# Performance work log

Measured on AMD Instinct MI355X. Metric: run time of the kernel, lower is better.

## Reference

```python
import jax, jax.numpy as jnp
import numpy as np
from jax import lax

C = 64
EPS = 1e-5


def _layernorm_c(x, g, b):
    # LayerNorm over channel dim of NCHW tensor (matches nn.LayerNorm([C]) applied on NHWC)
    mu = jnp.mean(x, axis=1, keepdims=True)
    var = jnp.var(x, axis=1, keepdims=True)
    xn = (x - mu) * lax.rsqrt(var + EPS)
    return xn * g[None, :, None, None] + b[None, :, None, None]


def _conv1x1(x, w, b):
    # w: [O, I]
    return jnp.einsum('bihw,oi->bohw', x, w) + b[None, :, None, None]


def _dwconv3x3(x, w, b):
    # depthwise 3x3, w: [C, 3, 3]
    k = w[:, None, :, :]  # OIHW with I=1
    y = lax.conv_general_dilated(x, k, (1, 1), 'SAME',
                                 feature_group_count=w.shape[0],
                                 dimension_numbers=('NCHW', 'OIHW', 'NCHW'))
    return y + b[None, :, None, None]


def setup_inputs() -> dict:
    key = jax.random.key(0)
    ks = jax.random.split(key, 24)
    s = 0.02
    d = {}
    d['x'] = jax.random.normal(ks[0], (4, C, 64, 64), dtype=jnp.float32)
    # CTA params
    d['cta_ln_g'] = jnp.ones((C,), jnp.float32)
    d['cta_ln_b'] = jnp.zeros((C,), jnp.float32)
    d['q_w'] = jax.random.normal(ks[1], (C, C), jnp.float32) * s
    d['q_b'] = jnp.zeros((C,), jnp.float32)
    d['k_w'] = jax.random.normal(ks[2], (C, 3, 3), jnp.float32) * s
    d['k_b'] = jnp.zeros((C,), jnp.float32)
    d['v_w'] = jax.random.normal(ks[3], (C, 3, 3), jnp.float32) * s
    d['v_b'] = jnp.zeros((C,), jnp.float32)
    d['cta_out_w'] = jax.random.normal(ks[4], (C, C), jnp.float32) * s
    d['cta_out_b'] = jnp.zeros((C,), jnp.float32)
    # NLE params
    d['nle_ln_g'] = jnp.ones((C,), jnp.float32)
    d['nle_ln_b'] = jnp.zeros((C,), jnp.float32)
    d['b1_w1'] = jax.random.normal(ks[5], (2 * C, C), jnp.float32) * s
    d['b1_b1'] = jnp.zeros((2 * C,), jnp.float32)
    d['b1_w2'] = jax.random.normal(ks[6], (2 * C, 3, 3), jnp.float32) * s
    d['b1_b2'] = jnp.zeros((2 * C,), jnp.float32)
    d['b2_w1'] = jax.random.normal(ks[7], (2 * C, C), jnp.float32) * s
    d['b2_b1'] = jnp.zeros((2 * C,), jnp.float32)
    d['b2_w2'] = jax.random.normal(ks[8], (2 * C, 3, 3), jnp.float32) * s
    d['b2_b2'] = jnp.zeros((2 * C,), jnp.float32)
    d['nle_out_w'] = jax.random.normal(ks[9], (C, 2 * C), jnp.float32) * s
    d['nle_out_b'] = jnp.zeros((C,), jnp.float32)
    return d


def csam_forward(x, cta_ln_g, cta_ln_b, q_w, q_b, k_w, k_b, v_w, v_b, cta_out_w, cta_out_b,
                 nle_ln_g, nle_ln_b, b1_w1, b1_b1, b1_w2, b1_b2, b2_w1, b2_b1, b2_w2, b2_b2,
                 nle_out_w, nle_out_b):
    B, Cc, H, W = x.shape
    scale = jnp.sqrt(jnp.float32(Cc))
    # --- CTA ---
    xn = _layernorm_c(x, cta_ln_g, cta_ln_b)
    q = _conv1x1(xn, q_w, q_b).reshape(B, Cc, H * W)      # [B,C,N]
    k = _dwconv3x3(xn, k_w, k_b).reshape(B, Cc, H * W)    # [B,C,N]
    v = _dwconv3x3(xn, v_w, v_b).reshape(B, Cc, H * W)    # [B,C,N]
    attn = jnp.einsum('bcn,bcm->bnm', q, k) / scale        # [B,N,N]
    attn = jax.nn.softmax(attn, axis=-1)
    out = jnp.einsum('bnm,bcm->bcn', attn, v).reshape(B, Cc, H, W)
    x_att = _conv1x1(out, cta_out_w, cta_out_b) + x
    # --- NLE ---
    xn2 = _layernorm_c(x_att, nle_ln_g, nle_ln_b)
    br1 = jax.nn.gelu(_dwconv3x3(_conv1x1(xn2, b1_w1, b1_b1), b1_w2, b1_b2), approximate=False)
    br2 = jax.nn.gelu(_dwconv3x3(_conv1x1(xn2, b2_w1, b2_b1), b2_w2, b2_b2), approximate=False)
    nle = _conv1x1(br1 * br2, nle_out_w, nle_out_b)
    return nle + x_att


def reference(x, cta_ln_g, cta_ln_b, q_w, q_b, k_w, k_b, v_w, v_b, cta_out_w, cta_out_b,
              nle_ln_g, nle_ln_b, b1_w1, b1_b1, b1_w2, b1_b2, b2_w1, b2_b1, b2_w2, b2_b2,
              nle_out_w, nle_out_b):
    return csam_forward(x, cta_ln_g, cta_ln_b, q_w, q_b, k_w, k_b, v_w, v_b, cta_out_w, cta_out_b,
                        nle_ln_g, nle_ln_b, b1_w1, b1_b1, b1_w2, b1_b2, b2_w1, b2_b1, b2_w2, b2_b2,
                        nle_out_w, nle_out_b)
```

## Files before the change

### kernel.cpp

```cpp
#include <hip/hip_runtime.h>
#include <hip/hip_bf16.h>
#include <math.h>

#define NPIX 4096
#define CH 64
#define BATCH 4
#define NSPLIT 4

typedef __attribute__((ext_vector_type(8))) short short8;
typedef __attribute__((ext_vector_type(4))) float f32x4;
typedef __attribute__((ext_vector_type(4))) unsigned short us4;
typedef __attribute__((ext_vector_type(4))) unsigned int u32x4;

static __device__ __forceinline__ unsigned short f2bf(float f) {
  union { float f; unsigned u; } v; v.f = f;
  unsigned u = v.u;
  unsigned r = u + 0x7FFF + ((u >> 16) & 1);
  return (unsigned short)(r >> 16);
}
static __device__ __forceinline__ float bf2f(unsigned short u) {
  union { unsigned u; float f; } v; v.u = ((unsigned)u) << 16; return v.f;
}
static __device__ __forceinline__ unsigned cvtpk(float lo, float hi) {
  unsigned r;
  asm("v_cvt_pk_bf16_f32 %0, %1, %2" : "=v"(r) : "v"(lo), "v"(hi));
  return r;
}

__global__ __launch_bounds__(256) void k_ln_q(
    const float* __restrict__ x, const float* __restrict__ lg, const float* __restrict__ lb,
    const float* __restrict__ qw, const float* __restrict__ qb,
    float* __restrict__ xn, unsigned short* __restrict__ Q)
{
  __shared__ float xT[64][64];
  __shared__ unsigned short xB[64][64];
  int tid = threadIdx.x, px = tid & 63, g4 = tid >> 6;
  int idx0 = blockIdx.x * 64;
  int idx = idx0 + px;
  int b = idx >> 12, p = idx & 4095;
  const float* xb = x + (size_t)b * CH * NPIX + p;
  for (int j = 0; j < 16; ++j) { int c = 16 * g4 + j; xT[c][px] = xb[(size_t)c * NPIX]; }
  __syncthreads();
  float xv[64]; float s = 0.f;
#pragma unroll
  for (int c = 0; c < 64; ++c) { xv[c] = xT[c][px]; s += xv[c]; }
  float mu = s * (1.f / 64.f), vs = 0.f;
#pragma unroll
  for (int c = 0; c < 64; ++c) { float d = xv[c] - mu; vs += d * d; }
  float rs = rsqrtf(vs * (1.f / 64.f) + 1e-5f);
#pragma unroll
  for (int c = 0; c < 64; ++c) xv[c] = (xv[c] - mu) * rs * lg[c] + lb[c];

  float* xnb = xn + (size_t)b * CH * NPIX + p;
#define LNQ_WR(C0)                                                             \
  {                                                                            \
    unsigned short t[16];                                                      \
    _Pragma("unroll") for (int j = 0; j < 16; ++j) {                           \
      float v = xv[C0 + j];                                                    \
      xnb[(size_t)(C0 + j) * NPIX] = v;                                        \
      t[j] = f2bf(v);                                                          \
    }                                                                          \
    *(short8*)&xB[px][(((C0 / 8) + 0) ^ (px & 7)) * 8] = *(short8*)t;          \
    *(short8*)&xB[px][(((C0 / 8) + 1) ^ (px & 7)) * 8] = *(short8*)(t + 8);    \
  }
  if (g4 == 0) LNQ_WR(0)
  else if (g4 == 1) LNQ_WR(16)
  else if (g4 == 2) LNQ_WR(32)
  else LNQ_WR(48)
#undef LNQ_WR
  __syncthreads();

  int lane = tid & 63, l15 = lane & 15, gg = lane >> 4;
  short8 af[2];
#pragma unroll
  for (int kc = 0; kc < 2; ++kc) {
    const float* wp = qw + (size_t)(g4 * 16 + l15) * 64 + kc * 32 + 8 * gg;
    unsigned short t[8];
#pragma unroll
    for (int j = 0; j < 8; ++j) t[j] = f2bf(wp[j]);
    af[kc] = *(short8*)t;
  }
  float bv[4];
#pragma unroll
  for (int r = 0; r < 4; ++r) bv[r] = qb[g4 * 16 + 4 * gg + r];
#pragma unroll
  for (int ct = 0; ct < 4; ++ct) {
    f32x4 acc = {bv[0], bv[1], bv[2], bv[3]};
    int row = ct * 16 + l15;
    short8 bf0 = *(const short8*)&xB[row][((0 + gg) ^ (row & 7)) * 8];
    short8 bf1 = *(const short8*)&xB[row][((4 + gg) ^ (row & 7)) * 8];
    acc = __builtin_amdgcn_mfma_f32_16x16x32_bf16(af[0], bf0, acc, 0, 0, 0);
    acc = __builtin_amdgcn_mfma_f32_16x16x32_bf16(af[1], bf1, acc, 0, 0, 0);
    us4 v;
#pragma unroll
    for (int r = 0; r < 4; ++r) v[r] = f2bf(acc[r] * 0.125f);
    *(us4*)(Q + (size_t)(idx0 + row) * 64 + g4 * 16 + 4 * gg) = v;
  }
}

__global__ __launch_bounds__(256) void k_dwkv(
    const float* __restrict__ xn,
    const float* __restrict__ kw, const float* __restrict__ kb,
    const float* __restrict__ vw, const float* __restrict__ vb,
    unsigned short* __restrict__ K, unsigned short* __restrict__ VT)
{
  int idx = blockIdx.x * 256 + threadIdx.x;
  int b = idx >> 12, p = idx & 4095;
  int h = p >> 6, w = p & 63;
  int c0 = blockIdx.y * 8;
  size_t base = (size_t)b * CH * NPIX;
  unsigned short kq[8];
#pragma unroll
  for (int j = 0; j < 8; ++j) {
    int c = c0 + j;
    const float* xc = xn + base + (size_t)c * NPIX;
    float ka = kb[c], va = vb[c];
#pragma unroll
    for (int dy = -1; dy <= 1; ++dy) {
#pragma unroll
      for (int dx = -1; dx <= 1; ++dx) {
        int hh = h + dy, ww = w + dx;
        float xvv = (hh >= 0 && hh < 64 && ww >= 0 && ww < 64) ? xc[hh * 64 + ww] : 0.f;
        int t = (dy + 1) * 3 + (dx + 1);
        ka += kw[c * 9 + t] * xvv;
        va += vw[c * 9 + t] * xvv;
      }
    }
    kq[j] = f2bf(ka);
    VT[((size_t)b * CH + c) * NPIX + p] = f2bf(va);
  }
  *(short8*)(K + (size_t)idx * 64 + c0) = *(short8*)(kq);
}

#define SW(r) ((((r) & 7) ^ (((r) >> 3) << 1)) & 7)
__global__ __launch_bounds__(256, 4) void k_attn(
    const unsigned short* __restrict__ Q, const unsigned short* __restrict__ K,
    const unsigned short* __restrict__ VT, unsigned short* __restrict__ OPb,
    float* __restrict__ LS)
{
  __shared__ unsigned short kls[2][64][64];
  __shared__ unsigned short vls[2][64][64];

  int tid = threadIdx.x;
  int wid = tid >> 6, lane = tid & 63;
  int l15 = lane & 15, g = lane >> 4;
  int b = blockIdx.y, split = blockIdx.z;
  int nbase = blockIdx.x * 64 + wid * 16;

  const unsigned short* Qb = Q + (size_t)b * NPIX * CH;
  const unsigned short* Kb = K + (size_t)b * NPIX * CH;
  const unsigned short* Vb = VT + (size_t)b * CH * NPIX;

  short8 qf0 = *(const short8*)(Qb + (size_t)(nbase + l15) * CH + 8 * g);
  short8 qf1 = *(const short8*)(Qb + (size_t)(nbase + l15) * CH + 32 + 8 * g);

  f32x4 acc[4];
#pragma unroll
  for (int i = 0; i < 4; ++i) acc[i] = (f32x4){0.f, 0.f, 0.f, 0.f};
  float lsum = 0.f;

  int srow = tid >> 3, sch = tid & 7;
  int srow1 = srow + 32;
  int wa0 = srow * 64 + ((sch ^ SW(srow)) * 8);
  int wa1 = srow1 * 64 + ((sch ^ SW(srow1)) * 8);
  const unsigned short* ksrc0 = Kb + (size_t)(split * 1024 + srow) * CH + sch * 8;
  const unsigned short* ksrc1 = Kb + (size_t)(split * 1024 + srow1) * CH + sch * 8;
  const unsigned short* vsrc0 = Vb + (size_t)srow * NPIX + split * 1024 + sch * 8;
  const unsigned short* vsrc1 = Vb + (size_t)srow1 * NPIX + split * 1024 + sch * 8;

  int kperm = 8 * (l15 >> 2) + (l15 & 3);

  short8 kg0, kg1, vg0, vg1;
  kg0 = *(const short8*)(ksrc0);
  kg1 = *(const short8*)(ksrc1);
  vg0 = *(const short8*)(vsrc0);
  vg1 = *(const short8*)(vsrc1);
  *(short8*)(&kls[0][0][0] + wa0) = kg0;
  *(short8*)(&kls[0][0][0] + wa1) = kg1;
  *(short8*)(&vls[0][0][0] + wa0) = vg0;
  *(short8*)(&vls[0][0][0] + wa1) = vg1;
  __syncthreads();

  for (int t = 0; t < 16; ++t) {
    if (t < 15) {
      int ko = (t + 1) * 64;
      kg0 = *(const short8*)(ksrc0 + (size_t)ko * CH);
      kg1 = *(const short8*)(ksrc1 + (size_t)ko * CH);
      vg0 = *(const short8*)(vsrc0 + ko);
      vg1 = *(const short8*)(vsrc1 + ko);
    }

    const unsigned short* kb = &kls[t & 1][0][0];
    const unsigned short* vb = &vls[t & 1][0][0];

#pragma unroll
    for (int s = 0; s < 2; ++s) {
      int r0 = s * 32 + kperm;
      int r1 = s * 32 + 4 + kperm;
      short8 kf00 = *(const short8*)(kb + r0 * 64 + (((0 + g) ^ SW(r0)) * 8));
      short8 kf01 = *(const short8*)(kb + r0 * 64 + (((4 + g) ^ SW(r0)) * 8));
      short8 kf10 = *(const short8*)(kb + r1 * 64 + (((0 + g) ^ SW(r1)) * 8));
      short8 kf11 = *(const short8*)(kb + r1 * 64 + (((4 + g) ^ SW(r1)) * 8));
      f32x4 s0 = {0.f, 0.f, 0.f, 0.f}, s1 = {0.f, 0.f, 0.f, 0.f};
      s0 = __builtin_amdgcn_mfma_f32_16x16x32_bf16(kf00, qf0, s0, 0, 0, 0);
      s0 = __builtin_amdgcn_mfma_f32_16x16x32_bf16(kf01, qf1, s0, 0, 0, 0);
      s1 = __builtin_amdgcn_mfma_f32_16x16x32_bf16(kf10, qf0, s1, 0, 0, 0);
      s1 = __builtin_amdgcn_mfma_f32_16x16x32_bf16(kf11, qf1, s1, 0, 0, 0);
      float p0 = __expf(s0[0]), p1 = __expf(s0[1]), p2 = __expf(s0[2]), p3 = __expf(s0[3]);
      float p4 = __expf(s1[0]), p5 = __expf(s1[1]), p6 = __expf(s1[2]), p7 = __expf(s1[3]);
      lsum += (p0 + p1) + (p2 + p3) + (p4 + p5) + (p6 + p7);
      u32x4 pk;
      pk[0] = cvtpk(p0, p1); pk[1] = cvtpk(p2, p3);
      pk[2] = cvtpk(p4, p5); pk[3] = cvtpk(p6, p7);
      short8 pb = *(short8*)&pk;
#pragma unroll
      for (int cs = 0; cs < 4; ++cs) {
        int row = cs * 16 + l15;
        short8 vf = *(const short8*)(vb + row * 64 + (((4 * s + g) ^ SW(row)) * 8));
        acc[cs] = __builtin_amdgcn_mfma_f32_16x16x32_bf16(vf, pb, acc[cs], 0, 0, 0);
      }
    }

    if (t < 15) {
      unsigned short* kw_ = &kls[(t + 1) & 1][0][0];
      unsigned short* vw_ = &vls[(t + 1) & 1][0][0];
      *(short8*)(kw_ + wa0) = kg0;
      *(short8*)(kw_ + wa1) = kg1;
      *(short8*)(vw_ + wa0) = vg0;
      *(short8*)(vw_ + wa1) = vg1;
    }
    __syncthreads();
  }

  lsum += __shfl_xor(lsum, 16, 64);
  lsum += __shfl_xor(lsum, 32, 64);

  size_t sb = ((size_t)split * BATCH + b) * NPIX;
  unsigned short* Ob = OPb + (sb + nbase + l15) * 64;
#pragma unroll
  for (int cs = 0; cs < 4; ++cs) {
    us4 v;
#pragma unroll
    for (int r = 0; r < 4; ++r) v[r] = f2bf(acc[cs][r]);
    *(us4*)(Ob + cs * 16 + 4 * g) = v;
  }
  if (g == 0) LS[sb + nbase + l15] = lsum;
}
#undef SW

__global__ __launch_bounds__(256) void k_reduce(
    const unsigned short* __restrict__ OPb, const float* __restrict__ LSv,
    unsigned short* __restrict__ AOT)
{
  int tid = threadIdx.x;
  size_t e0 = (size_t)blockIdx.x * 4096;
#pragma unroll
  for (int h = 0; h < 2; ++h) {
    int off = (h * 256 + tid) * 8;
    int pix = blockIdx.x * 64 + (off >> 6);
    float sv[8] = {0.f, 0.f, 0.f, 0.f, 0.f, 0.f, 0.f, 0.f};
    float ls = 0.f;
#pragma unroll
    for (int sp = 0; sp < NSPLIT; ++sp) {
      short8 a = *(const short8*)(OPb + (size_t)sp * BATCH * NPIX * 64 + e0 + off);
#pragma unroll
      for (int j = 0; j < 8; ++j) sv[j] += bf2f((unsigned short)a[j]);
      ls += LSv[(size_t)sp * BATCH * NPIX + pix];
    }
    float inv = 1.f / ls;
    unsigned short t[8];
#pragma unroll
    for (int j = 0; j < 8; ++j) t[j] = f2bf(sv[j] * inv);
    *(short8*)(AOT + e0 + off) = *(short8*)t;
  }
}

__global__ __launch_bounds__(256) void k_proj_ln2(
    const unsigned short* __restrict__ AOT, const float* __restrict__ x,
    const float* __restrict__ ow, const float* __restrict__ ob,
    const float* __restrict__ lg, const float* __restrict__ lb,
    float* __restrict__ xatt, unsigned short* __restrict__ xn2T)
{
  __shared__ float sm1[4][4][16], sm2[4][4][16];
  int tid = threadIdx.x;
  int wid = tid >> 6, lane = tid & 63;
  int l15 = lane & 15, g = lane >> 4;
  int b = blockIdx.y, pxb = blockIdx.x * 64;
  const unsigned short* In = AOT + ((size_t)b * NPIX + pxb) * 64;

  short8 af[2];
#pragma unroll
  for (int kc = 0; kc < 2; ++kc) {
    const float* wp = ow + (size_t)(wid * 16 + l15) * 64 + kc * 32 + 8 * g;
    unsigned short t[8];
#pragma unroll
    for (int j = 0; j < 8; ++j) t[j] = f2bf(wp[j]);
    af[kc] = *(short8*)t;
  }
  float bv[4], lgv[4], lbv[4];
#pragma unroll
  for (int r = 0; r < 4; ++r) {
    int o = wid * 16 + 4 * g + r;
    bv[r] = ob[o]; lgv[r] = lg[o]; lbv[r] = lb[o];
  }
  f32x4 acc[4];
#pragma unroll
  for (int ct = 0; ct < 4; ++ct) acc[ct] = (f32x4){bv[0], bv[1], bv[2], bv[3]};
#pragma unroll
  for (int ct = 0; ct < 4; ++ct) {
    short8 bf0 = *(const short8*)(In + (size_t)(ct * 16 + l15) * 64 + 8 * g);
    short8 bf1 = *(const short8*)(In + (size_t)(ct * 16 + l15) * 64 + 32 + 8 * g);
    acc[ct] = __builtin_amdgcn_mfma_f32_16x16x32_bf16(af[0], bf0, acc[ct], 0, 0, 0);
    acc[ct] = __builtin_amdgcn_mfma_f32_16x16x32_bf16(af[1], bf1, acc[ct], 0, 0, 0);
  }

  float xo[4][4];
#pragma unroll
  for (int ct = 0; ct < 4; ++ct) {
    int p = pxb + ct * 16 + l15;
    float s1 = 0.f, s2 = 0.f;
#pragma unroll
    for (int r = 0; r < 4; ++r) {
      int o = wid * 16 + 4 * g + r;
      size_t oi = ((size_t)b * CH + o) * NPIX + p;
      float v = acc[ct][r] + x[oi];
      xatt[oi] = v;
      xo[ct][r] = v;
      s1 += v; s2 += v * v;
    }
    s1 += __shfl_xor(s1, 16, 64); s1 += __shfl_xor(s1, 32, 64);
    s2 += __shfl_xor(s2, 16, 64); s2 += __shfl_xor(s2, 32, 64);
    if (g == 0) { sm1[wid][ct][l15] = s1; sm2[wid][ct][l15] = s2; }
  }
  __syncthreads();
#pragma unroll
  for (int ct = 0; ct < 4; ++ct) {
    int p = pxb + ct * 16 + l15;
    float mu = (sm1[0][ct][l15] + sm1[1][ct][l15] + sm1[2][ct][l15] + sm1[3][ct][l15]) * (1.f / 64.f);
    float ms = (sm2[0][ct][l15] + sm2[1][ct][l15] + sm2[2][ct][l15] + sm2[3][ct][l15]) * (1.f / 64.f);
    float rs = rsqrtf(ms - mu * mu + 1e-5f);
    us4 v4;
#pragma unroll
    for (int r = 0; r < 4; ++r) v4[r] = f2bf((xo[ct][r] - mu) * rs * lgv[r] + lbv[r]);
    *(us4*)(xn2T + ((size_t)b * NPIX + p) * 64 + wid * 16 + 4 * g) = v4;
  }
}

__global__ __launch_bounds__(256) void k_pw_both(
    const unsigned short* __restrict__ xn2T,
    const float* __restrict__ w1, const float* __restrict__ bb1,
    const float* __restrict__ w2, const float* __restrict__ bb2,
    float* __restrict__ t1, float* __restrict__ t2)
{
  int tid = threadIdx.x;
  int wid = tid >> 6, lane = tid & 63;
  int l15 = lane & 15, g = lane >> 4;
  int b = blockIdx.y, pxb = blockIdx.x * 64;
  const unsigned short* In = xn2T + ((size_t)b * NPIX + pxb) * 64;
  const float* W  = (wid & 2) ? w2 : w1;
  const float* bb = (wid & 2) ? bb2 : bb1;
  float* t        = (wid & 2) ? t2 : t1;
  int oh = (wid & 1) * 64;

  short8 af[4][2];
#pragma unroll
  for (int ot = 0; ot < 4; ++ot)
#pragma unroll
    for (int kc = 0; kc < 2; ++kc) {
      const float* wp = W + (size_t)(oh + ot * 16 + l15) * 64 + kc * 32 + 8 * g;
      unsigned short tt[8];
#pragma unroll
      for (int j = 0; j < 8; ++j) tt[j] = f2bf(wp[j]);
      af[ot][kc] = *(short8*)tt;
    }
  f32x4 acc[4][4];
#pragma unroll
  for (int ot = 0; ot < 4; ++ot) {
    float b0 = bb[oh + ot * 16 + 4 * g + 0];
    float b1 = bb[oh + ot * 16 + 4 * g + 1];
    float b2 = bb[oh + ot * 16 + 4 * g + 2];
    float b3 = bb[oh + ot * 16 + 4 * g + 3];
#pragma unroll
    for (int ct = 0; ct < 4; ++ct) acc[ot][ct] = (f32x4){b0, b1, b2, b3};
  }
#pragma unroll
  for (int ct = 0; ct < 4; ++ct) {
    short8 bf0 = *(const short8*)(In + (size_t)(ct * 16 + l15) * 64 + 8 * g);
    short8 bf1 = *(const short8*)(In + (size_t)(ct * 16 + l15) * 64 + 32 + 8 * g);
#pragma unroll
    for (int ot = 0; ot < 4; ++ot) {
      acc[ot][ct] = __builtin_amdgcn_mfma_f32_16x16x32_bf16(af[ot][0], bf0, acc[ot][ct], 0, 0, 0);
      acc[ot][ct] = __builtin_amdgcn_mfma_f32_16x16x32_bf16(af[ot][1], bf1, acc[ot][ct], 0, 0, 0);
    }
  }
#pragma unroll
  for (int ot = 0; ot < 4; ++ot)
#pragma unroll
    for (int ct = 0; ct < 4; ++ct) {
      int p = pxb + ct * 16 + l15;
#pragma unroll
      for (int r = 0; r < 4; ++r) {
        int o = oh + ot * 16 + 4 * g + r;
        t[((size_t)b * 128 + o) * NPIX + p] = acc[ot][ct][r];
      }
    }
}

__global__ __launch_bounds__(256) void k_dwgelu(
    const float* __restrict__ t1, const float* __restrict__ t2,
    const float* __restrict__ w1, const float* __restrict__ bb1,
    const float* __restrict__ w2, const float* __restrict__ bb2,
    unsigned short* __restrict__ g12T)
{
  int idx = blockIdx.x * 256 + threadIdx.x;
  int b = idx >> 12, p = idx & 4095;
  int h = p >> 6, w = p & 63;
  int c0 = blockIdx.y * 8;
  unsigned short outv[8];
#pragma unroll
  for (int j = 0; j < 8; ++j) {
    int c = c0 + j;
    size_t tb = ((size_t)b * 128 + c) * NPIX;
    float a1 = bb1[c], a2 = bb2[c];
#pragma unroll
    for (int dy = -1; dy <= 1; ++dy) {
#pragma unroll
      for (int dx = -1; dx <= 1; ++dx) {
        int hh = h + dy, ww = w + dx;
        bool ok = (hh >= 0 && hh < 64 && ww >= 0 && ww < 64);
        float v1 = ok ? t1[tb + hh * 64 + ww] : 0.f;
        float v2 = ok ? t2[tb + hh * 64 + ww] : 0.f;
        int t = (dy + 1) * 3 + (dx + 1);
        a1 += w1[c * 9 + t] * v1;
        a2 += w2[c * 9 + t] * v2;
      }
    }
    float ge1 = 0.5f * a1 * (1.f + erff(a1 * 0.70710678118654752f));
    float ge2 = 0.5f * a2 * (1.f + erff(a2 * 0.70710678118654752f));
    outv[j] = f2bf(ge1 * ge2);
  }
  *(short8*)(g12T + (size_t)idx * 128 + c0) = *(short8*)outv;
}

__global__ __launch_bounds__(256) void k_out(
    const float* __restrict__ W, const float* __restrict__ bias,
    const unsigned short* __restrict__ InT, const float* __restrict__ res,
    float* __restrict__ outF)
{
  int tid = threadIdx.x;
  int wid = tid >> 6, lane = tid & 63;
  int l15 = lane & 15, g = lane >> 4;
  int b = blockIdx.y, pxb = blockIdx.x * 64;
  const unsigned short* In = InT + ((size_t)b * NPIX + pxb) * 128;

  short8 af[4];
#pragma unroll
  for (int kc = 0; kc < 4; ++kc) {
    const float* wp = W + (size_t)(wid * 16 + l15) * 128 + kc * 32 + 8 * g;
    unsigned short t[8];
#pragma unroll
    for (int j = 0; j < 8; ++j) t[j] = f2bf(wp[j]);
    af[kc] = *(short8*)t;
  }
  float bv[4];
#pragma unroll
  for (int r = 0; r < 4; ++r) bv[r] = bias[wid * 16 + 4 * g + r];
#pragma unroll
  for (int ct = 0; ct < 4; ++ct) {
    f32x4 acc = {bv[0], bv[1], bv[2], bv[3]};
#pragma unroll
    for (int kc = 0; kc < 4; ++kc) {
      short8 bf = *(const short8*)(In + (size_t)(ct * 16 + l15) * 128 + kc * 32 + 8 * g);
      acc = __builtin_amdgcn_mfma_f32_16x16x32_bf16(af[kc], bf, acc, 0, 0, 0);
    }
    int p = pxb + ct * 16 + l15;
#pragma unroll
    for (int r = 0; r < 4; ++r) {
      int o = wid * 16 + 4 * g + r;
      size_t oi = ((size_t)b * CH + o) * NPIX + p;
      outF[oi] = acc[r] + res[oi];
    }
  }
}

extern "C" void kernel_launch(void* const* d_in, const int* in_sizes, int n_in,
                              void* d_out, int out_size, void* d_ws, size_t ws_size,
                              hipStream_t stream) {
  const float* x        = (const float*)d_in[0];
  const float* cta_ln_g = (const float*)d_in[1];
  const float* cta_ln_b = (const float*)d_in[2];
  const float* q_w      = (const float*)d_in[3];
  const float* q_b      = (const float*)d_in[4];
  const float* k_w      = (const float*)d_in[5];
  const float* k_b      = (const float*)d_in[6];
  const float* v_w      = (const float*)d_in[7];
  const float* v_b      = (const float*)d_in[8];
  const float* cta_out_w= (const float*)d_in[9];
  const float* cta_out_b= (const float*)d_in[10];
  const float* nle_ln_g = (const float*)d_in[11];
  const float* nle_ln_b = (const float*)d_in[12];
  const float* b1_w1    = (const float*)d_in[13];
  const float* b1_b1    = (const float*)d_in[14];
  const float* b1_w2    = (const float*)d_in[15];
  const float* b1_b2    = (const float*)d_in[16];
  const float* b2_w1    = (const float*)d_in[17];
  const float* b2_b1    = (const float*)d_in[18];
  const float* b2_w2    = (const float*)d_in[19];
  const float* b2_b2    = (const float*)d_in[20];
  const float* nle_out_w= (const float*)d_in[21];
  const float* nle_out_b= (const float*)d_in[22];

  char* ws = (char*)d_ws;
  float*          xn   = (float*)(ws);
  unsigned short* Qb   = (unsigned short*)(ws + (4u  << 20));
  unsigned short* Kb   = (unsigned short*)(ws + (6u  << 20));
  unsigned short* VTb  = (unsigned short*)(ws + (8u  << 20));
  unsigned short* OPb  = (unsigned short*)(ws + (10u << 20));
  float*          LSb  = (float*)(ws + (18u << 20));
  unsigned short* AOT  = (unsigned short*)(ws + (19u << 20));
  float*          xatt = (float*)(ws + (21u << 20));
  unsigned short* xn2T = (unsigned short*)(ws + (25u << 20));
  float*          t1   = (float*)(ws + (27u << 20));
  float*          t2   = (float*)(ws + (35u << 20));
  unsigned short* g12T = (unsigned short*)(ws);

  k_ln_q     <<<256, 256, 0, stream>>>(x, cta_ln_g, cta_ln_b, q_w, q_b, xn, Qb);
  k_dwkv     <<<dim3(64, 8), 256, 0, stream>>>(xn, k_w, k_b, v_w, v_b, Kb, VTb);
  k_attn     <<<dim3(64, BATCH, NSPLIT), 256, 0, stream>>>(Qb, Kb, VTb, OPb, LSb);
  k_reduce   <<<256, 256, 0, stream>>>(OPb, LSb, AOT);
  k_proj_ln2 <<<dim3(64, 4), 256, 0, stream>>>(AOT, x, cta_out_w, cta_out_b, nle_ln_g, nle_ln_b, xatt, xn2T);
  k_pw_both  <<<dim3(64, 4), 256, 0, stream>>>(xn2T, b1_w1, b1_b1, b2_w1, b2_b1, t1, t2);
  k_dwgelu   <<<dim3(64, 16), 256, 0, stream>>>(t1, t2, b1_w2, b1_b2, b2_w2, b2_b2, g12T);
  k_out      <<<dim3(64, 4), 256, 0, stream>>>(nle_out_w, nle_out_b, g12T, xatt, (float*)d_out);
}
```

Before: 76.52 us.

## Fuse split-attention reduce into projection, store pointwise outputs as bf16, halve tiles

Result: slower. 96.33 us (+25.9%).

```diff
diff --git a/kernel.cpp b/kernel.cpp
--- a/kernel.cpp
+++ b/kernel.cpp
@@ -248,45 +248,42 @@
 }
 #undef SW
 
-__global__ __launch_bounds__(256) void k_reduce(
+__global__ __launch_bounds__(256) void k_proj_ln2(
     const unsigned short* __restrict__ OPb, const float* __restrict__ LSv,
-    unsigned short* __restrict__ AOT)
-{
-  int tid = threadIdx.x;
-  size_t e0 = (size_t)blockIdx.x * 4096;
-#pragma unroll
-  for (int h = 0; h < 2; ++h) {
-    int off = (h * 256 + tid) * 8;
-    int pix = blockIdx.x * 64 + (off >> 6);
-    float sv[8] = {0.f, 0.f, 0.f, 0.f, 0.f, 0.f, 0.f, 0.f};
-    float ls = 0.f;
-#pragma unroll
-    for (int sp = 0; sp < NSPLIT; ++sp) {
-      short8 a = *(const short8*)(OPb + (size_t)sp * BATCH * NPIX * 64 + e0 + off);
-#pragma unroll
-      for (int j = 0; j < 8; ++j) sv[j] += bf2f((unsigned short)a[j]);
-      ls += LSv[(size_t)sp * BATCH * NPIX + pix];
-    }
-    float inv = 1.f / ls;
-    unsigned short t[8];
-#pragma unroll
-    for (int j = 0; j < 8; ++j) t[j] = f2bf(sv[j] * inv);
-    *(short8*)(AOT + e0 + off) = *(short8*)t;
-  }
-}
-
-__global__ __launch_bounds__(256) void k_proj_ln2(
-    const unsigned short* __restrict__ AOT, const float* __restrict__ x,
+    const float* __restrict__ x,
     const float* __restrict__ ow, const float* __restrict__ ob,
     const float* __restrict__ lg, const float* __restrict__ lb,
     float* __restrict__ xatt, unsigned short* __restrict__ xn2T)
 {
+  __shared__ unsigned short aT[64][64];
   __shared__ float sm1[4][4][16], sm2[4][4][16];
   int tid = threadIdx.x;
+  int b = blockIdx.y, pxb = blockIdx.x * 64;
+
+#pragma unroll
+  for (int h = 0; h < 2; ++h) {
+    int off = (h * 256 + tid) * 8;
+    int px = off >> 6;
+    float sv[8] = {0.f, 0.f, 0.f, 0.f, 0.f, 0.f, 0.f, 0.f};
+    float ls = 0.f;
+#pragma unroll
+    for (int sp = 0; sp < NSPLIT; ++sp) {
+      size_t sbase = ((size_t)(sp * BATCH + b) * NPIX + pxb);
+      short8 a = *(const short8*)(OPb + sbase * 64 + off);
+#pragma unroll
+      for (int j = 0; j < 8; ++j) sv[j] += bf2f((unsigned short)a[j]);
+      ls += LSv[sbase + px];
+    }
+    float inv = 1.f / ls;
+    unsigned short t[8];
+#pragma unroll
+    for (int j = 0; j < 8; ++j) t[j] = f2bf(sv[j] * inv);
+    *(short8*)&aT[px][(((tid & 7) ^ (px & 7)) * 8)] = *(short8*)t;
+  }
+  __syncthreads();
+
   int wid = tid >> 6, lane = tid & 63;
   int l15 = lane & 15, g = lane >> 4;
-  int b = blockIdx.y, pxb = blockIdx.x * 64;
-  const unsigned short* In = AOT + ((size_t)b * NPIX + pxb) * 64;
 
   short8 af[2];
 #pragma unroll
@@ -308,8 +305,9 @@
   for (int ct = 0; ct < 4; ++ct) acc[ct] = (f32x4){bv[0], bv[1], bv[2], bv[3]};
 #pragma unroll
   for (int ct = 0; ct < 4; ++ct) {
-    short8 bf0 = *(const short8*)(In + (size_t)(ct * 16 + l15) * 64 + 8 * g);
-    short8 bf1 = *(const short8*)(In + (size_t)(ct * 16 + l15) * 64 + 32 + 8 * g);
+    int row = ct * 16 + l15;
+    short8 bf0 = *(const short8*)&aT[row][(((0 + g) ^ (row & 7)) * 8)];
+    short8 bf1 = *(const short8*)&aT[row][(((4 + g) ^ (row & 7)) * 8)];
     acc[ct] = __builtin_amdgcn_mfma_f32_16x16x32_bf16(af[0], bf0, acc[ct], 0, 0, 0);
     acc[ct] = __builtin_amdgcn_mfma_f32_16x16x32_bf16(af[1], bf1, acc[ct], 0, 0, 0);
   }
@@ -350,16 +348,16 @@
     const unsigned short* __restrict__ xn2T,
     const float* __restrict__ w1, const float* __restrict__ bb1,
     const float* __restrict__ w2, const float* __restrict__ bb2,
-    float* __restrict__ t1, float* __restrict__ t2)
+    unsigned short* __restrict__ t1, unsigned short* __restrict__ t2)
 {
   int tid = threadIdx.x;
   int wid = tid >> 6, lane = tid & 63;
   int l15 = lane & 15, g = lane >> 4;
-  int b = blockIdx.y, pxb = blockIdx.x * 64;
+  int b = blockIdx.y, pxb = blockIdx.x * 32;
   const unsigned short* In = xn2T + ((size_t)b * NPIX + pxb) * 64;
   const float* W  = (wid & 2) ? w2 : w1;
   const float* bb = (wid & 2) ? bb2 : bb1;
-  float* t        = (wid & 2) ? t2 : t1;
+  unsigned short* t = (wid & 2) ? t2 : t1;
   int oh = (wid & 1) * 64;
 
   short8 af[4][2];
@@ -373,7 +371,7 @@
       for (int j = 0; j < 8; ++j) tt[j] = f2bf(wp[j]);
       af[ot][kc] = *(short8*)tt;
     }
-  f32x4 acc[4][4];
+  f32x4 acc[4][2];
 #pragma unroll
   for (int ot = 0; ot < 4; ++ot) {
     float b0 = bb[oh + ot * 16 + 4 * g + 0];
@@ -381,10 +379,10 @@
     float b2 = bb[oh + ot * 16 + 4 * g + 2];
     float b3 = bb[oh + ot * 16 + 4 * g + 3];
 #pragma unroll
-    for (int ct = 0; ct < 4; ++ct) acc[ot][ct] = (f32x4){b0, b1, b2, b3};
-  }
-#pragma unroll
-  for (int ct = 0; ct < 4; ++ct) {
+    for (int ct = 0; ct < 2; ++ct) acc[ot][ct] = (f32x4){b0, b1, b2, b3};
+  }
+#pragma unroll
+  for (int ct = 0; ct < 2; ++ct) {
     short8 bf0 = *(const short8*)(In + (size_t)(ct * 16 + l15) * 64 + 8 * g);
     short8 bf1 = *(const short8*)(In + (size_t)(ct * 16 + l15) * 64 + 32 + 8 * g);
 #pragma unroll
@@ -396,18 +394,18 @@
 #pragma unroll
   for (int ot = 0; ot < 4; ++ot)
 #pragma unroll
-    for (int ct = 0; ct < 4; ++ct) {
+    for (int ct = 0; ct < 2; ++ct) {
       int p = pxb + ct * 16 + l15;
 #pragma unroll
       for (int r = 0; r < 4; ++r) {
         int o = oh + ot * 16 + 4 * g + r;
-        t[((size_t)b * 128 + o) * NPIX + p] = acc[ot][ct][r];
+        t[((size_t)b * 128 + o) * NPIX + p] = f2bf(acc[ot][ct][r]);
       }
     }
 }
 
 __global__ __launch_bounds__(256) void k_dwgelu(
-    const float* __restrict__ t1, const float* __restrict__ t2,
+    const unsigned short* __restrict__ t1, const unsigned short* __restrict__ t2,
     const float* __restrict__ w1, const float* __restrict__ bb1,
     const float* __restrict__ w2, const float* __restrict__ bb2,
     unsigned short* __restrict__ g12T)
@@ -428,8 +426,8 @@
       for (int dx = -1; dx <= 1; ++dx) {
         int hh = h + dy, ww = w + dx;
         bool ok = (hh >= 0 && hh < 64 && ww >= 0 && ww < 64);
-        float v1 = ok ? t1[tb + hh * 64 + ww] : 0.f;
-        float v2 = ok ? t2[tb + hh * 64 + ww] : 0.f;
+        float v1 = ok ? bf2f(t1[tb + hh * 64 + ww]) : 0.f;
+        float v2 = ok ? bf2f(t2[tb + hh * 64 + ww]) : 0.f;
         int t = (dy + 1) * 3 + (dx + 1);
         a1 += w1[c * 9 + t] * v1;
         a2 += w2[c * 9 + t] * v2;
@@ -450,7 +448,7 @@
   int tid = threadIdx.x;
   int wid = tid >> 6, lane = tid & 63;
   int l15 = lane & 15, g = lane >> 4;
-  int b = blockIdx.y, pxb = blockIdx.x * 64;
+  int b = blockIdx.y, pxb = blockIdx.x * 32;
   const unsigned short* In = InT + ((size_t)b * NPIX + pxb) * 128;
 
   short8 af[4];
@@ -466,7 +464,7 @@
 #pragma unroll
   for (int r = 0; r < 4; ++r) bv[r] = bias[wid * 16 + 4 * g + r];
 #pragma unroll
-  for (int ct = 0; ct < 4; ++ct) {
+  for (int ct = 0; ct < 2; ++ct) {
     f32x4 acc = {bv[0], bv[1], bv[2], bv[3]};
 #pragma unroll
     for (int kc = 0; kc < 4; ++kc) {
@@ -517,19 +515,17 @@
   unsigned short* VTb  = (unsigned short*)(ws + (8u  << 20));
   unsigned short* OPb  = (unsigned short*)(ws + (10u << 20));
   float*          LSb  = (float*)(ws + (18u << 20));
-  unsigned short* AOT  = (unsigned short*)(ws + (19u << 20));
   float*          xatt = (float*)(ws + (21u << 20));
   unsigned short* xn2T = (unsigned short*)(ws + (25u << 20));
-  float*          t1   = (float*)(ws + (27u << 20));
-  float*          t2   = (float*)(ws + (35u << 20));
+  unsigned short* t1   = (unsigned short*)(ws + (27u << 20));
+  unsigned short* t2   = (unsigned short*)(ws + (31u << 20));
   unsigned short* g12T = (unsigned short*)(ws);
 
   k_ln_q     <<<256, 256, 0, stream>>>(x, cta_ln_g, cta_ln_b, q_w, q_b, xn, Qb);
   k_dwkv     <<<dim3(64, 8), 256, 0, stream>>>(xn, k_w, k_b, v_w, v_b, Kb, VTb);
   k_attn     <<<dim3(64, BATCH, NSPLIT), 256, 0, stream>>>(Qb, Kb, VTb, OPb, LSb);
-  k_reduce   <<<256, 256, 0, stream>>>(OPb, LSb, AOT);
-  k_proj_ln2 <<<dim3(64, 4), 256, 0, stream>>>(AOT, x, cta_out_w, cta_out_b, nle_ln_g, nle_ln_b, xatt, xn2T);
-  k_pw_both  <<<dim3(64, 4), 256, 0, stream>>>(xn2T, b1_w1, b1_b1, b2_w1, b2_b1, t1, t2);
+  k_proj_ln2 <<<dim3(64, 4), 256, 0, stream>>>(OPb, LSb, x, cta_out_w, cta_out_b, nle_ln_g, nle_ln_b, xatt, xn2T);
+  k_pw_both  <<<dim3(128, 4), 256, 0, stream>>>(xn2T, b1_w1, b1_b1, b2_w1, b2_b1, t1, t2);
   k_dwgelu   <<<dim3(64, 16), 256, 0, stream>>>(t1, t2, b1_w2, b1_b2, b2_w2, b2_b2, g12T);
-  k_out      <<<dim3(64, 4), 256, 0, stream>>>(nle_out_w, nle_out_b, g12T, xatt, (float*)d_out);
-}
+  k_out      <<<dim3(128, 4), 256, 0, stream>>>(nle_out_w, nle_out_b, g12T, xatt, (float*)d_out);
+}
```
